# Kernel tuning notes

Hardware: AMD Instinct MI355X
Metric: run time of the kernel (lower is better)

Reference implementation:

```python
import jax, jax.numpy as jnp
import numpy as np
from functools import partial

RED = 128      # reduced_dim
MK = 24        # r2d_m * r2d_k
HD, WD = 32, 16  # depth feature grid after 3 stride-2 convs on 256x128


def _conv(x, w, b):
    # torch Conv2d(k=3, stride=2, padding=1), NCHW / OIHW
    y = jax.lax.conv_general_dilated(
        x, w, window_strides=(2, 2), padding=((1, 1), (1, 1)),
        dimension_numbers=("NCHW", "OIHW", "NCHW"))
    return y + b[None, :, None, None]


def setup_inputs() -> dict:
    key = jax.random.key(0)
    ks = jax.random.split(key, 24)
    B = 64
    s = 0.02
    inp = {
        "features": jax.random.normal(ks[0], (B, 129, 768), jnp.float32),
        "d": jax.random.uniform(ks[1], (B, 1, 256, 128), jnp.float32),
        "W_rg": jax.random.normal(ks[2], (768, RED), jnp.float32) * s,
        "b_rg": jnp.zeros((RED,), jnp.float32),
        "W_rl": jax.random.normal(ks[3], (768, RED), jnp.float32) * s,
        "b_rl": jnp.zeros((RED,), jnp.float32),
        "conv1_w": jax.random.normal(ks[4], (64, 1, 3, 3), jnp.float32) * s,
        "conv1_b": jnp.zeros((64,), jnp.float32),
        "conv2_w": jax.random.normal(ks[5], (128, 64, 3, 3), jnp.float32) * s,
        "conv2_b": jnp.zeros((128,), jnp.float32),
        "conv3_w": jax.random.normal(ks[6], (128, 128, 3, 3), jnp.float32) * s,
        "conv3_b": jnp.zeros((128,), jnp.float32),
        "g_depth": jax.random.normal(ks[7], (RED,), jnp.float32),
        "W_merge": jax.random.normal(ks[8], (2 * RED, RED), jnp.float32) * s,
        "b_merge": jnp.zeros((RED,), jnp.float32),
        "W_q": jax.random.normal(ks[9], (2 * RED, RED), jnp.float32) * s,
        "b_q": jnp.zeros((RED,), jnp.float32),
        "W_v": jax.random.normal(ks[10], (RED, RED), jnp.float32) * s,
        "b_v": jnp.zeros((RED,), jnp.float32),
        "W_sel": jax.random.normal(ks[11], (RED, 3 * MK), jnp.float32) * s,
        "b_sel": jnp.zeros((3 * MK,), jnp.float32),
        "W_cls": jax.random.normal(ks[12], (RED, 751), jnp.float32) * s,
    }
    return inp


def _forward(features, d, W_rg, b_rg, W_rl, b_rl, conv1_w, conv1_b, conv2_w,
             conv2_b, conv3_w, conv3_b, g_depth, W_merge, b_merge, W_q, b_q,
             W_v, b_v, W_sel, b_sel, W_cls):
    B = features.shape[0]
    N = features.shape[1] - 1
    global_feat = features[:, 0] @ W_rg + b_rg                 # (B, 128)
    local_feat = features[:, 1:] @ W_rl + b_rl                 # (B, N, 128)
    lcg = jnp.concatenate(
        [jnp.broadcast_to(global_feat[:, None], (B, N, RED)), local_feat], -1)

    dep = _conv(_conv(_conv(d, conv1_w, conv1_b), conv2_w, conv2_b),
                conv3_w, conv3_b)                              # (B,128,32,16)
    dep = dep.transpose(0, 2, 3, 1).reshape(B, HD * WD, RED)
    lcgd = jnp.concatenate(
        [jnp.broadcast_to(g_depth[None, None], (B, HD * WD, RED)), dep], -1)
    lcgd = lcgd @ W_merge + b_merge

    q = lcg @ W_q + b_q                                        # (B,N,128)
    v = lcgd @ W_v + b_v                                       # (B,512,128)
    sel = jax.nn.sigmoid(q @ W_sel + b_sel)                    # (B,N,72)
    lx = sel[:, :, 0:2 * MK:2]                                 # (B,N,24)
    ly = sel[:, :, 1:2 * MK:2]
    attn = jax.nn.softmax(sel[:, :, 2 * MK:], axis=-1)

    # integer corner grid (original uses // stride == floor(loc*(dim-1)))
    x1 = jnp.floor(lx * (WD - 1))
    x2 = jnp.minimum(x1 + 1.0, float(WD - 1))
    y1 = jnp.floor(ly * (HD - 1))
    y2 = jnp.minimum(y1 + 1.0, float(HD - 1))
    xi1, xi2 = x1.astype(jnp.int32), x2.astype(jnp.int32)
    yi1, yi2 = y1.astype(jnp.int32), y2.astype(jnp.int32)

    # faithful to original gather: index = x_idx * Wd + y_idx
    gather = jax.vmap(lambda vb, ib: vb[ib])                   # (512,C),(N,K)->(N,K,C)
    f0 = gather(v, xi1 * WD + yi2)
    f1 = gather(v, xi2 * WD + yi2)
    f2 = gather(v, xi2 * WD + yi1)
    f3 = gather(v, xi1 * WD + yi1)

    # query coordinates scaled by full grid size (as in the original)
    x = lx * WD
    y = ly * HD
    w_ = x2 - x1
    h_ = y2 - y1
    degenerate = (h_ == 0) | (w_ == 0)
    denom = jnp.where(h_ * w_ == 0, 1.0, h_ * w_)
    coeff = jnp.where(degenerate, 2.0, 1.0 / denom)            # (B,N,24)
    xv0 = jnp.where(w_ == 0, 1.0, x2 - x)
    xv1 = jnp.where(w_ == 0, 1.0, x - x1)
    yv0 = jnp.where(h_ == 0, 1.0, y2 - y)
    yv1 = jnp.where(h_ == 0, 1.0, y - y1)

    # xv^T @ [[f0,f1],[f2,f3]] @ yv, per channel
    interp = coeff[..., None] * (
        xv0[..., None] * (f0 * yv0[..., None] + f1 * yv1[..., None]) +
        xv1[..., None] * (f2 * yv0[..., None] + f3 * yv1[..., None]))

    r2d_feat = jnp.mean(interp * attn[..., None], axis=-2)     # (B,N,128)
    final_embedding = jnp.mean(r2d_feat, axis=1)               # (B,128)
    cls_score = final_embedding @ W_cls                        # (B,751)
    return cls_score, final_embedding


def reference(features, d, W_rg, b_rg, W_rl, b_rl, conv1_w, conv1_b, conv2_w,
              conv2_b, conv3_w, conv3_b, g_depth, W_merge, b_merge, W_q, b_q,
              W_v, b_v, W_sel, b_sel, W_cls):
    return _forward(features, d, W_rg, b_rg, W_rl, b_rl, conv1_w, conv1_b,
                    conv2_w, conv2_b, conv3_w, conv3_b, g_depth, W_merge,
                    b_merge, W_q, b_q, W_v, b_v, W_sel, b_sel, W_cls)
```

## Files before the change

### kernel.cpp

```cpp
#include <hip/hip_runtime.h>
#include <hip/hip_bf16.h>


typedef __attribute__((ext_vector_type(8))) short short8;
typedef __attribute__((ext_vector_type(4))) short shortx4;
typedef __attribute__((ext_vector_type(4))) float floatx4;
typedef __attribute__((ext_vector_type(4))) int intx4;

#define MFMA16(a, b, c) __builtin_amdgcn_mfma_f32_16x16x32_bf16(a, b, c, 0, 0, 0)

__global__ __launch_bounds__(256) void prep_a(
    const float* __restrict__ W_q, const float* __restrict__ W_sel,
    const float* __restrict__ W_merge, const float* __restrict__ W_v,
    const float* __restrict__ g_depth, const float* __restrict__ b_merge,
    const float* __restrict__ features, const float* __restrict__ W_rg,
    const float* __restrict__ b_rg, const float* __restrict__ c2w,
    const float* __restrict__ c3w,
    float* __restrict__ W_qs, float* __restrict__ W_mv,
    float* __restrict__ c0, float* __restrict__ gfeat,
    __hip_bfloat16* __restrict__ w2t, __hip_bfloat16* __restrict__ w3t)
{
    __shared__ float fr_s[768];
    int bid = blockIdx.x, t = threadIdx.x;
    if (bid < 72) {
        int j = bid;
        float acc = 0.f;
        for (int k = 0; k < 128; ++k)
            acc = fmaf(W_q[t * 128 + k], W_sel[k * 72 + j], acc);
        W_qs[t * 72 + j] = acc;
    } else if (bid < 200) {
        int j = bid - 72;
        if (t < 128) {
            float acc = 0.f;
            for (int k = 0; k < 128; ++k)
                acc = fmaf(W_merge[(128 + t) * 128 + k], W_v[k * 128 + j], acc);
            W_mv[t * 128 + j] = acc;
        }
    } else if (bid == 200) {
        if (t < 128) {
            float acc = b_merge[t];
            for (int k = 0; k < 128; ++k)
                acc = fmaf(g_depth[k], W_merge[k * 128 + t], acc);
            c0[t] = acc;
        }
    } else if (bid < 265) {
        int row = bid - 201;
        for (int l = t; l < 768; l += 256)
            fr_s[l] = features[(long)row * 129 * 768 + l];
        __syncthreads();
        if (t < 128) {
            float acc = b_rg[t];
            for (int k = 0; k < 768; ++k)
                acc = fmaf(fr_s[k], W_rg[k * 128 + t], acc);
            gfeat[row * 128 + t] = acc;
        }
    } else if (bid < 553) {
        int idx = (bid - 265) * 256 + t;
        if (idx < 128 * 576) {
            int oc = idx / 576, k = idx % 576;
            int s = k >> 6, ic = k & 63;
            w2t[idx] = __float2bfloat16(c2w[oc * 576 + ic * 9 + s]);
        }
    } else {
        int idx = (bid - 553) * 256 + t;
        if (idx < 128 * 1152) {
            int oc = idx / 1152, k = idx % 1152;
            int s = k >> 7, ic = k & 127;
            w3t[idx] = __float2bfloat16(c3w[oc * 1152 + ic * 9 + s]);
        }
    }
}

__global__ __launch_bounds__(256) void prep2_k(
    const float* __restrict__ W_rl, const float* __restrict__ W_qs,
    const float* __restrict__ W_sel, const float* __restrict__ b_rl,
    const float* __restrict__ b_q, const float* __restrict__ b_sel,
    const float* __restrict__ gfeat, const float* __restrict__ c0,
    const float* __restrict__ W_v, const float* __restrict__ b_v,
    float* __restrict__ W_big, float* __restrict__ rowbias,
    float* __restrict__ c0v)
{
    int bid = blockIdx.x, t = threadIdx.x;
    if (bid < 216) {
        int j = bid / 3;
        int i = (bid % 3) * 256 + t;
        float acc = 0.f;
        for (int k = 0; k < 128; ++k)
            acc = fmaf(W_rl[i * 128 + k], W_qs[(128 + k) * 72 + j], acc);
        W_big[i * 72 + j] = acc;
    } else if (bid < 288) {
        int j = bid - 216;
        if (t < 64) {
            float vb = b_sel[j];
            for (int k = 0; k < 128; ++k) {
                vb = fmaf(b_rl[k], W_qs[(128 + k) * 72 + j], vb);
                vb = fmaf(b_q[k], W_sel[k * 72 + j], vb);
            }
            float acc = vb;
            for (int k = 0; k < 128; ++k)
                acc = fmaf(gfeat[t * 128 + k], W_qs[k * 72 + j], acc);
            rowbias[t * 72 + j] = acc;
        }
    } else {
        if (t < 128) {
            float acc = b_v[t];
            for (int k = 0; k < 128; ++k)
                acc = fmaf(c0[k], W_v[k * 128 + t], acc);
            c0v[t] = acc;
        }
    }
}

__global__ __launch_bounds__(256) void prep_b(
    const float* __restrict__ W_mv, const float* __restrict__ W_big,
    __hip_bfloat16* __restrict__ Bh, __hip_bfloat16* __restrict__ Bl,
    __hip_bfloat16* __restrict__ Wbh, __hip_bfloat16* __restrict__ Wbl)
{
    int bid = blockIdx.x, t = threadIdx.x;
    if (bid < 64) {
        int idx = bid * 256 + t;
        int n = idx >> 7, k = idx & 127;
        float w = W_mv[k * 128 + n];
        __hip_bfloat16 h = __float2bfloat16(w);
        Bh[idx] = h;
        Bl[idx] = __float2bfloat16(w - __bfloat162float(h));
    } else {
        int idx = (bid - 64) * 256 + t;
        if (idx < 80 * 768) {
            int n = idx / 768, k = idx - n * 768;
            float w = (n < 72) ? W_big[k * 72 + n] : 0.f;
            __hip_bfloat16 h = __float2bfloat16(w);
            Wbh[idx] = h;
            Wbl[idx] = __float2bfloat16(w - __bfloat162float(h));
        }
    }
}

__global__ __launch_bounds__(256) void conv1_k(
    const float* __restrict__ d, const float* __restrict__ w,
    const float* __restrict__ bias, __hip_bfloat16* __restrict__ out)
{
    __shared__ float in_s[3][66];
    __shared__ float ws_[576];
    __shared__ float bs_[64];
    int tid = threadIdx.x;
    int owhalf = blockIdx.x & 1;
    int oh = (blockIdx.x >> 1) & 127;
    int b  = blockIdx.x >> 8;
    int owbase = owhalf * 32;

    for (int l = tid; l < 576; l += 256) ws_[l] = w[l];
    if (tid < 64) bs_[tid] = bias[tid];
    for (int l = tid; l < 3 * 66; l += 256) {
        int r = l / 66, c = l % 66;
        int ih = 2 * oh - 1 + r;
        int iw = 2 * owbase - 1 + c;
        float v = 0.f;
        if ((unsigned)ih < 256u && (unsigned)iw < 128u)
            v = d[(b * 256 + ih) * 128 + iw];
        in_s[r][c] = v;
    }
    __syncthreads();

    int owl = tid >> 3, ocg = tid & 7;
    float in9[9];
#pragma unroll
    for (int r = 0; r < 3; ++r)
#pragma unroll
        for (int c = 0; c < 3; ++c)
            in9[r * 3 + c] = in_s[r][2 * owl + c];

    short8 res;
#pragma unroll
    for (int j = 0; j < 8; ++j) {
        int oc = ocg * 8 + j;
        float a = bs_[oc];
#pragma unroll
        for (int s = 0; s < 9; ++s) a = fmaf(in9[s], ws_[oc * 9 + s], a);
        union { __hip_bfloat16 h; short s; } u;
        u.h = __float2bfloat16(a);
        res[j] = u.s;
    }
    long pos = ((long)(b * 128 + oh) * 64 + owbase + owl);
    *(short8*)((short*)out + pos * 64 + ocg * 8) = res;
}

__global__ __launch_bounds__(256) void conv2_mfma(
    const __hip_bfloat16* __restrict__ in, const __hip_bfloat16* __restrict__ w2t,
    const float* __restrict__ bias, __hip_bfloat16* __restrict__ out)
{
    __shared__ short A_lds[128][72];
    __shared__ short B_lds[128][72];
    int tid = threadIdx.x;
    int oh0 = blockIdx.x * 4;
    int b   = blockIdx.y;
    int lane = tid & 63, wave = tid >> 6;
    int l16 = lane & 15, lh = lane >> 4;
    const short* inp = (const short*)in;
    const short* w2p = (const short*)w2t;

    floatx4 acc[2][8] = {};

    for (int s = 0; s < 9; ++s) {
        int kh = s / 3, kw = s - kh * 3;
        short8 av[4], bv[4];
#pragma unroll
        for (int i = 0; i < 4; ++i) {
            int c = tid + i * 256;
            int pos = c >> 3, seg = c & 7;
            int ohl = pos >> 5, ow = pos & 31;
            int ih = 2 * (oh0 + ohl) - 1 + kh;
            int iw = 2 * ow - 1 + kw;
            short8 v = {0,0,0,0,0,0,0,0};
            if ((unsigned)ih < 128u && (unsigned)iw < 64u)
                v = *(const short8*)(inp + (((long)(b * 128 + ih) * 64 + iw) * 64 + seg * 8));
            av[i] = v;
            bv[i] = *(const short8*)(w2p + pos * 576 + s * 64 + seg * 8);
        }
        __syncthreads();
#pragma unroll
        for (int i = 0; i < 4; ++i) {
            int c = tid + i * 256;
            int pos = c >> 3, seg = c & 7;
            *(short8*)&A_lds[pos][seg * 8] = av[i];
            *(short8*)&B_lds[pos][seg * 8] = bv[i];
        }
        __syncthreads();
#pragma unroll
        for (int half = 0; half < 2; ++half) {
            short8 a0 = *(const short8*)&A_lds[wave * 32 + l16][half * 32 + lh * 8];
            short8 a1 = *(const short8*)&A_lds[wave * 32 + 16 + l16][half * 32 + lh * 8];
#pragma unroll
            for (int ni = 0; ni < 8; ++ni) {
                short8 bvf = *(const short8*)&B_lds[ni * 16 + l16][half * 32 + lh * 8];
                acc[0][ni] = MFMA16(a0, bvf, acc[0][ni]);
                acc[1][ni] = MFMA16(a1, bvf, acc[1][ni]);
            }
        }
    }

    float bf[8];
#pragma unroll
    for (int ni = 0; ni < 8; ++ni) bf[ni] = bias[ni * 16 + l16];
#pragma unroll
    for (int mi = 0; mi < 2; ++mi)
#pragma unroll
        for (int r = 0; r < 4; ++r) {
            int m = wave * 32 + mi * 16 + lh * 4 + r;
            int ohl = m >> 5, ow = m & 31;
            __hip_bfloat16* op = out + (((long)(b * 64 + oh0 + ohl) * 32) + ow) * 128;
#pragma unroll
            for (int ni = 0; ni < 8; ++ni) {
                int oc = ni * 16 + l16;
                op[oc] = __float2bfloat16(acc[mi][ni][r] + bf[ni]);
            }
        }
}

__global__ __launch_bounds__(256) void conv3_mfma(
    const __hip_bfloat16* __restrict__ in, const __hip_bfloat16* __restrict__ w3t,
    const float* __restrict__ bias, float* __restrict__ dep)
{
    __shared__ short A_lds[64][136];
    __shared__ short B_lds[128][136];
    int tid = threadIdx.x;
    int oh0 = blockIdx.x * 4;
    int b   = blockIdx.y;
    int lane = tid & 63, wave = tid >> 6;
    int wr = wave >> 1, wc = wave & 1;
    int l16 = lane & 15, lh = lane >> 4;
    const short* inp = (const short*)in;
    const short* w3p = (const short*)w3t;

    floatx4 acc[2][4] = {};

    for (int s = 0; s < 9; ++s) {
        int kh = s / 3, kw = s - kh * 3;
        short8 av[4], bv[8];
#pragma unroll
        for (int i = 0; i < 4; ++i) {
            int c = tid + i * 256;
            int pos = c >> 4, seg = c & 15;
            int oa = pos >> 4, ow = pos & 15;
            int ih = 2 * (oh0 + oa) - 1 + kh;
            int iw = 2 * ow - 1 + kw;
            short8 v = {0,0,0,0,0,0,0,0};
            if ((unsigned)ih < 64u && (unsigned)iw < 32u)
                v = *(const short8*)(inp + (((long)(b * 64 + ih) * 32 + iw) * 128 + seg * 8));
            av[i] = v;
        }
#pragma unroll
        for (int i = 0; i < 8; ++i) {
            int c = tid + i * 256;
            int oc = c >> 4, seg = c & 15;
            bv[i] = *(const short8*)(w3p + oc * 1152 + s * 128 + seg * 8);
        }
        __syncthreads();
#pragma unroll
        for (int i = 0; i < 4; ++i) {
            int c = tid + i * 256;
            int pos = c >> 4, seg = c & 15;
            *(short8*)&A_lds[pos][seg * 8] = av[i];
        }
#pragma unroll
        for (int i = 0; i < 8; ++i) {
            int c = tid + i * 256;
            int oc = c >> 4, seg = c & 15;
            *(short8*)&B_lds[oc][seg * 8] = bv[i];
        }
        __syncthreads();
#pragma unroll
        for (int ks = 0; ks < 4; ++ks) {
            short8 a0 = *(const short8*)&A_lds[wr * 32 + l16][ks * 32 + lh * 8];
            short8 a1 = *(const short8*)&A_lds[wr * 32 + 16 + l16][ks * 32 + lh * 8];
#pragma unroll
            for (int ni = 0; ni < 4; ++ni) {
                short8 bvf = *(const short8*)&B_lds[wc * 64 + ni * 16 + l16][ks * 32 + lh * 8];
                acc[0][ni] = MFMA16(a0, bvf, acc[0][ni]);
                acc[1][ni] = MFMA16(a1, bvf, acc[1][ni]);
            }
        }
    }

    float bf[4];
#pragma unroll
    for (int ni = 0; ni < 4; ++ni) bf[ni] = bias[wc * 64 + ni * 16 + l16];
#pragma unroll
    for (int mi = 0; mi < 2; ++mi)
#pragma unroll
        for (int r = 0; r < 4; ++r) {
            int m = wr * 32 + mi * 16 + lh * 4 + r;
            int oa2 = m >> 4, ow2 = m & 15;
            float* op = dep + ((long)b * 512 + (oh0 + oa2) * 16 + ow2) * 128;
#pragma unroll
            for (int ni = 0; ni < 4; ++ni) {
                int oc = wc * 64 + ni * 16 + l16;
                op[oc] = acc[mi][ni][r] + bf[ni];
            }
        }
}

__global__ __launch_bounds__(256) void vgemm_mfma(
    const float* __restrict__ dep, const __hip_bfloat16* __restrict__ Bh,
    const __hip_bfloat16* __restrict__ Bl, const float* __restrict__ c0v,
    float* __restrict__ v)
{
    __shared__ short Ah[64][136];
    __shared__ short Al[64][136];
    int tid = threadIdx.x;
    int m0 = blockIdx.x * 64;

    for (int l4 = tid; l4 < 64 * 32; l4 += 256) {
        int r = l4 >> 5, c4 = l4 & 31;
        const float* sp = dep + ((long)(m0 + r) << 7) + c4 * 4;
        shortx4 hv, lv;
#pragma unroll
        for (int i = 0; i < 4; ++i) {
            float f = sp[i];
            union { __hip_bfloat16 b; short s; } uh, ul;
            uh.b = __float2bfloat16(f);
            ul.b = __float2bfloat16(f - __bfloat162float(uh.b));
            hv[i] = uh.s; lv[i] = ul.s;
        }
        *(shortx4*)&Ah[r][c4 * 4] = hv;
        *(shortx4*)&Al[r][c4 * 4] = lv;
    }
    __syncthreads();

    int lane = tid & 63, wave = tid >> 6;
    int wr = wave >> 1, wc = wave & 1;
    int l16 = lane & 15, lh = lane >> 4;
    floatx4 acc[2][4] = {};
#pragma unroll
    for (int kk = 0; kk < 4; ++kk) {
        short8 ah[2], al[2];
#pragma unroll
        for (int mi = 0; mi < 2; ++mi) {
            ah[mi] = *(const short8*)&Ah[wr * 32 + mi * 16 + l16][kk * 32 + lh * 8];
            al[mi] = *(const short8*)&Al[wr * 32 + mi * 16 + l16][kk * 32 + lh * 8];
        }
#pragma unroll
        for (int nf = 0; nf < 4; ++nf) {
            int gn = wc * 64 + nf * 16 + l16;
            short8 bh = *(const short8*)((const short*)Bh + gn * 128 + kk * 32 + lh * 8);
            short8 bl = *(const short8*)((const short*)Bl + gn * 128 + kk * 32 + lh * 8);
#pragma unroll
            for (int mi = 0; mi < 2; ++mi) {
                acc[mi][nf] = MFMA16(ah[mi], bh, acc[mi][nf]);
                acc[mi][nf] = MFMA16(al[mi], bh, acc[mi][nf]);
                acc[mi][nf] = MFMA16(ah[mi], bl, acc[mi][nf]);
            }
        }
    }
#pragma unroll
    for (int nf = 0; nf < 4; ++nf) {
        int gn = wc * 64 + nf * 16 + l16;
        float cv = c0v[gn];
#pragma unroll
        for (int mi = 0; mi < 2; ++mi)
#pragma unroll
            for (int r = 0; r < 4; ++r) {
                int m = m0 + wr * 32 + mi * 16 + lh * 4 + r;
                v[(long)m * 128 + gn] = acc[mi][nf][r] + cv;
            }
    }
}

__global__ __launch_bounds__(256) void selbw_k(
    const float* __restrict__ F, const __hip_bfloat16* __restrict__ Wbh,
    const __hip_bfloat16* __restrict__ Wbl, const float* __restrict__ rowbias,
    int* __restrict__ idxb, float* __restrict__ wtb)
{
    __shared__ short Ah[16][136];
    __shared__ short Al[16][136];
    __shared__ float slx[16][24], sly[16][24], satt[16][24];
    int tid = threadIdx.x;
    int m0 = blockIdx.x * 16;
    int padd = (m0 >> 7) + 1;
    int lane = tid & 63, wave = tid >> 6;
    int l16 = lane & 15, lh = lane >> 4;

    int sr = tid >> 4, sc = (tid & 15) * 8;
    const float* fsrc = F + (long)(m0 + sr + padd) * 768 + sc;

    floatx4 acc0 = {0.f, 0.f, 0.f, 0.f};
    floatx4 acc1 = {0.f, 0.f, 0.f, 0.f};
    bool two = (wave == 3);
    const short* bhp = (const short*)Wbh;
    const short* blp = (const short*)Wbl;
    int gn0 = wave * 16 + l16;
    int gn1 = 64 + l16;

    for (int c = 0; c < 6; ++c) {
        __syncthreads();
        float4 f0 = *(const float4*)(fsrc + c * 128);
        float4 f1 = *(const float4*)(fsrc + c * 128 + 4);
        shortx4 h0, l0, h1, l1;
#pragma unroll
        for (int i = 0; i < 4; ++i) {
            union { __hip_bfloat16 b; short s; } uh, ul;
            float fa = (&f0.x)[i];
            uh.b = __float2bfloat16(fa);
            ul.b = __float2bfloat16(fa - __bfloat162float(uh.b));
            h0[i] = uh.s; l0[i] = ul.s;
            float fb = (&f1.x)[i];
            uh.b = __float2bfloat16(fb);
            ul.b = __float2bfloat16(fb - __bfloat162float(uh.b));
            h1[i] = uh.s; l1[i] = ul.s;
        }
        *(shortx4*)&Ah[sr][sc]     = h0;
        *(shortx4*)&Ah[sr][sc + 4] = h1;
        *(shortx4*)&Al[sr][sc]     = l0;
        *(shortx4*)&Al[sr][sc + 4] = l1;
        __syncthreads();
#pragma unroll
        for (int ks = 0; ks < 4; ++ks) {
            short8 ah = *(const short8*)&Ah[l16][ks * 32 + lh * 8];
            short8 al = *(const short8*)&Al[l16][ks * 32 + lh * 8];
            int koff = c * 128 + ks * 32 + lh * 8;
            short8 bh0 = *(const short8*)(bhp + gn0 * 768 + koff);
            short8 bl0 = *(const short8*)(blp + gn0 * 768 + koff);
            acc0 = MFMA16(ah, bh0, acc0);
            acc0 = MFMA16(al, bh0, acc0);
            acc0 = MFMA16(ah, bl0, acc0);
            if (two) {
                short8 bh1 = *(const short8*)(bhp + gn1 * 768 + koff);
                short8 bl1 = *(const short8*)(blp + gn1 * 768 + koff);
                acc1 = MFMA16(ah, bh1, acc1);
                acc1 = MFMA16(al, bh1, acc1);
                acc1 = MFMA16(ah, bl1, acc1);
            }
        }
    }

    if (wave < 3) {
        int j = wave * 16 + l16;
#pragma unroll
        for (int r = 0; r < 4; ++r) {
            int rl = lh * 4 + r;
            float val = acc0[r] + rowbias[((m0 + rl) >> 7) * 72 + j];
            float sg = 1.f / (1.f + expf(-val));
            if (j & 1) sly[rl][j >> 1] = sg;
            else       slx[rl][j >> 1] = sg;
        }
    } else {
#pragma unroll
        for (int r = 0; r < 4; ++r) {
            int rl = lh * 4 + r;
            int b72 = ((m0 + rl) >> 7) * 72;
            float s0 = 1.f / (1.f + expf(-(acc0[r] + rowbias[b72 + 48 + l16])));
            float s1 = -1e30f;
            if (l16 < 8)
                s1 = 1.f / (1.f + expf(-(acc1[r] + rowbias[b72 + 64 + l16])));
            float mx = fmaxf(s0, s1);
#pragma unroll
            for (int s = 1; s < 16; s <<= 1)
                mx = fmaxf(mx, __shfl_xor(mx, s));
            float e0 = expf(s0 - mx);
            float e1 = (l16 < 8) ? expf(s1 - mx) : 0.f;
            float sum = e0 + e1;
#pragma unroll
            for (int s = 1; s < 16; s <<= 1)
                sum += __shfl_xor(sum, s);
            satt[rl][l16] = e0 / sum;
            if (l16 < 8) satt[rl][16 + l16] = e1 / sum;
        }
    }
    __syncthreads();

    for (int e = tid; e < 384; e += 256) {
        int rl = e / 24, k = e - rl * 24;
        int row = m0 + rl;
        float lxv = slx[rl][k], lyv = sly[rl][k];
        float a = satt[rl][k] * (1.f / 24.f);
        float x1 = floorf(lxv * 15.f), x2 = fminf(x1 + 1.f, 15.f);
        float y1 = floorf(lyv * 31.f), y2 = fminf(y1 + 1.f, 31.f);
        int xi1 = (int)x1, xi2 = (int)x2, yi1 = (int)y1, yi2 = (int)y2;
        float x = lxv * 16.f, y = lyv * 32.f;
        float w_ = x2 - x1, h_ = y2 - y1;
        float hwp = h_ * w_;
        bool deg = (h_ == 0.f) || (w_ == 0.f);
        float denom = (hwp == 0.f) ? 1.f : hwp;
        float coeff = (deg ? 2.f : 1.f / denom) * a;
        float xv0 = (w_ == 0.f) ? 1.f : (x2 - x);
        float xv1 = (w_ == 0.f) ? 1.f : (x - x1);
        float yv0 = (h_ == 0.f) ? 1.f : (y2 - y);
        float yv1 = (h_ == 0.f) ? 1.f : (y - y1);
        intx4 iv; floatx4 wv;
        iv[0] = (xi1 * 16 + yi2) * 128;
        iv[1] = (xi2 * 16 + yi2) * 128;
        iv[2] = (xi2 * 16 + yi1) * 128;
        iv[3] = (xi1 * 16 + yi1) * 128;
        wv[0] = coeff * xv0 * yv0;
        wv[1] = coeff * xv0 * yv1;
        wv[2] = coeff * xv1 * yv0;
        wv[3] = coeff * xv1 * yv1;
        *(intx4*)&idxb[(long)row * 96 + k * 4] = iv;
        *(floatx4*)&wtb[(long)row * 96 + k * 4] = wv;
    }
}

__global__ __launch_bounds__(256) void r2d_k(
    const float* __restrict__ v, const int* __restrict__ idxb,
    const float* __restrict__ wtb, float* __restrict__ r2d)
{
    int rg = blockIdx.x;
    int b  = blockIdx.y;
    int tid = threadIdx.x;
    int c  = tid & 127;
    int rp = tid >> 7;
    __shared__ int sidx[8][96];
    __shared__ float swt[8][96];
    for (int l = tid; l < 8 * 96; l += 256) {
        int rr = l / 96, e = l - rr * 96;
        long base = ((long)(b * 128 + rg * 8 + rr)) * 96 + e;
        sidx[rr][e] = idxb[base];
        swt[rr][e]  = wtb[base];
    }
    __syncthreads();
    const float* vb = v + (long)b * 512 * 128 + c;
#pragma unroll
    for (int it = 0; it < 4; ++it) {
        int rr = it * 2 + rp;
        const int* si = sidx[rr];
        const float* sw = swt[rr];
        float acc = 0.f;
#pragma unroll
        for (int k = 0; k < 24; ++k) {
            float v0 = vb[si[k * 4 + 0]];
            float v1 = vb[si[k * 4 + 1]];
            float v2 = vb[si[k * 4 + 2]];
            float v3 = vb[si[k * 4 + 3]];
            acc = fmaf(sw[k * 4 + 0], v0, acc);
            acc = fmaf(sw[k * 4 + 1], v1, acc);
            acc = fmaf(sw[k * 4 + 2], v2, acc);
            acc = fmaf(sw[k * 4 + 3], v3, acc);
        }
        r2d[((long)(b * 128 + rg * 8 + rr)) * 128 + c] = acc;
    }
}

__global__ __launch_bounds__(256) void fecls_k(
    const float* __restrict__ r2d, const float* __restrict__ W_cls,
    float* __restrict__ out)
{
    __shared__ float fe_s[128];
    int b = blockIdx.x, t = threadIdx.x;
    if (t < 128) {
        float acc = 0.f;
        for (int nn = 0; nn < 128; ++nn)
            acc += r2d[((long)b * 128 + nn) * 128 + t];
        acc *= (1.f / 128.f);
        fe_s[t] = acc;
        out[64 * 751 + b * 128 + t] = acc;
    }
    __syncthreads();
    for (int j = t; j < 751; j += 256) {
        float acc = 0.f;
        for (int k = 0; k < 128; ++k)
            acc = fmaf(fe_s[k], W_cls[k * 751 + j], acc);
        out[b * 751 + j] = acc;
    }
}

extern "C" void kernel_launch(void* const* d_in, const int* in_sizes, int n_in,
                              void* d_out, int out_size, void* d_ws, size_t ws_size,
                              hipStream_t stream)
{
    const float* features = (const float*)d_in[0];
    const float* d        = (const float*)d_in[1];
    const float* W_rg  = (const float*)d_in[2];
    const float* b_rg  = (const float*)d_in[3];
    const float* W_rl  = (const float*)d_in[4];
    const float* b_rl  = (const float*)d_in[5];
    const float* c1w   = (const float*)d_in[6];
    const float* c1b   = (const float*)d_in[7];
    const float* c2w   = (const float*)d_in[8];
    const float* c2b   = (const float*)d_in[9];
    const float* c3w   = (const float*)d_in[10];
    const float* c3b   = (const float*)d_in[11];
    const float* g_depth = (const float*)d_in[12];
    const float* W_merge = (const float*)d_in[13];
    const float* b_merge = (const float*)d_in[14];
    const float* W_q   = (const float*)d_in[15];
    const float* b_q   = (const float*)d_in[16];
    const float* W_v   = (const float*)d_in[17];
    const float* b_v   = (const float*)d_in[18];
    const float* W_sel = (const float*)d_in[19];
    const float* b_sel = (const float*)d_in[20];
    const float* W_cls = (const float*)d_in[21];
    float* out = (float*)d_out;

    char* ws = (char*)d_ws;
    __hip_bfloat16* c1 = (__hip_bfloat16*)(ws + 0);
    float* dep    = (float*)(ws + 0);
    float* v      = (float*)(ws + 33554432);
    __hip_bfloat16* c2 = (__hip_bfloat16*)(ws + 67108864);
    __hip_bfloat16* w2t = (__hip_bfloat16*)(ws + 100663296);
    __hip_bfloat16* w3t = (__hip_bfloat16*)(ws + 100810752);
    float* W_qs    = (float*)(ws + 101105664);
    float* W_mv    = (float*)(ws + 101179392);
    float* W_big   = (float*)(ws + 101244928);
    float* rowbias = (float*)(ws + 101466112);
    float* c0b     = (float*)(ws + 101484544);
    float* c0v     = (float*)(ws + 101485056);
    float* gfeat   = (float*)(ws + 101485568);
    __hip_bfloat16* Wmv_bh = (__hip_bfloat16*)(ws + 101518336);
    __hip_bfloat16* Wmv_bl = (__hip_bfloat16*)(ws + 101551104);
    __hip_bfloat16* Wbig_h = (__hip_bfloat16*)(ws + 101583872);
    __hip_bfloat16* Wbig_l = (__hip_bfloat16*)(ws + 101706752);
    int*   idxb   = (int*)(ws + 101832704);
    float* wtb    = (float*)(ws + 104978432);
    float* r2d    = (float*)(ws + 113836544);

    prep_a<<<1129, 256, 0, stream>>>(W_q, W_sel, W_merge, W_v, g_depth, b_merge,
                                     features, W_rg, b_rg, c2w, c3w,
                                     W_qs, W_mv, c0b, gfeat, w2t, w3t);
    prep2_k<<<289, 256, 0, stream>>>(W_rl, W_qs, W_sel, b_rl, b_q, b_sel,
                                     gfeat, c0b, W_v, b_v, W_big, rowbias, c0v);
    prep_b<<<304, 256, 0, stream>>>(W_mv, W_big, Wmv_bh, Wmv_bl, Wbig_h, Wbig_l);

    conv1_k<<<16384, 256, 0, stream>>>(d, c1w, c1b, c1);
    conv2_mfma<<<dim3(16, 64), 256, 0, stream>>>(c1, w2t, c2b, c2);
    conv3_mfma<<<dim3(8, 64), 256, 0, stream>>>(c2, w3t, c3b, dep);

    vgemm_mfma<<<512, 256, 0, stream>>>(dep, Wmv_bh, Wmv_bl, c0v, v);
    selbw_k<<<512, 256, 0, stream>>>(features, Wbig_h, Wbig_l, rowbias,
                                     idxb, wtb);

    r2d_k<<<dim3(16, 64), 256, 0, stream>>>(v, idxb, wtb, r2d);
    fecls_k<<<64, 256, 0, stream>>>(r2d, W_cls, out);
}
```

Measured before the change: 215.9 us.

## Fuse value GEMM into conv3 epilogue and retile conv1 over four rows

The conv3 kernel now writes its biased output into LDS as bf16 hi/lo pairs and runs the split-precision value GEMM on that tile directly, so the separate vgemm kernel and the 32 MB fp32 depth-feature round trip through global memory go away. Separately, conv1 now handles four output rows across the full width per block (2048 blocks instead of 16384), which amortizes the weight and bias staging and reduces block count. The price is longer conv3 blocks with more register pressure and an extra barrier, and conv1 threads that each compute eight positions.

```diff
diff --git a/kernel.cpp b/kernel.cpp
--- a/kernel.cpp
+++ b/kernel.cpp
@@ -140,21 +140,20 @@
     const float* __restrict__ d, const float* __restrict__ w,
     const float* __restrict__ bias, __hip_bfloat16* __restrict__ out)
 {
-    __shared__ float in_s[3][66];
+    __shared__ float in_s[9][130];
     __shared__ float ws_[576];
     __shared__ float bs_[64];
     int tid = threadIdx.x;
-    int owhalf = blockIdx.x & 1;
-    int oh = (blockIdx.x >> 1) & 127;
-    int b  = blockIdx.x >> 8;
-    int owbase = owhalf * 32;
+    int ohg = blockIdx.x & 31;
+    int b   = blockIdx.x >> 5;
+    int oh0 = ohg * 4;
 
     for (int l = tid; l < 576; l += 256) ws_[l] = w[l];
     if (tid < 64) bs_[tid] = bias[tid];
-    for (int l = tid; l < 3 * 66; l += 256) {
-        int r = l / 66, c = l % 66;
-        int ih = 2 * oh - 1 + r;
-        int iw = 2 * owbase - 1 + c;
+    for (int l = tid; l < 9 * 130; l += 256) {
+        int r = l / 130, c = l - r * 130;
+        int ih = 2 * oh0 - 1 + r;
+        int iw = c - 1;
         float v = 0.f;
         if ((unsigned)ih < 256u && (unsigned)iw < 128u)
             v = d[(b * 256 + ih) * 128 + iw];
@@ -162,27 +161,29 @@
     }
     __syncthreads();
 
-    int owl = tid >> 3, ocg = tid & 7;
-    float in9[9];
-#pragma unroll
-    for (int r = 0; r < 3; ++r)
-#pragma unroll
-        for (int c = 0; c < 3; ++c)
-            in9[r * 3 + c] = in_s[r][2 * owl + c];
-
-    short8 res;
-#pragma unroll
-    for (int j = 0; j < 8; ++j) {
-        int oc = ocg * 8 + j;
-        float a = bs_[oc];
-#pragma unroll
-        for (int s = 0; s < 9; ++s) a = fmaf(in9[s], ws_[oc * 9 + s], a);
-        union { __hip_bfloat16 h; short s; } u;
-        u.h = __float2bfloat16(a);
-        res[j] = u.s;
-    }
-    long pos = ((long)(b * 128 + oh) * 64 + owbase + owl);
-    *(short8*)((short*)out + pos * 64 + ocg * 8) = res;
+    int ocg = tid & 7;
+#pragma unroll
+    for (int pb = 0; pb < 8; ++pb) {
+        int pos = pb * 32 + (tid >> 3);
+        int ohl = pos >> 6, ow = pos & 63;
+        short8 res;
+#pragma unroll
+        for (int j = 0; j < 8; ++j) {
+            int oc = ocg * 8 + j;
+            float a = bs_[oc];
+#pragma unroll
+            for (int kh = 0; kh < 3; ++kh)
+#pragma unroll
+                for (int kw = 0; kw < 3; ++kw)
+                    a = fmaf(in_s[2 * ohl + kh][2 * ow + kw],
+                             ws_[oc * 9 + kh * 3 + kw], a);
+            union { __hip_bfloat16 h; short s; } u;
+            u.h = __float2bfloat16(a);
+            res[j] = u.s;
+        }
+        long gpos = ((long)(b * 128 + oh0 + ohl) * 64 + ow);
+        *(short8*)((short*)out + gpos * 64 + ocg * 8) = res;
+    }
 }
 
 __global__ __launch_bounds__(256) void conv2_mfma(
@@ -259,7 +260,9 @@
 
 __global__ __launch_bounds__(256) void conv3_mfma(
     const __hip_bfloat16* __restrict__ in, const __hip_bfloat16* __restrict__ w3t,
-    const float* __restrict__ bias, float* __restrict__ dep)
+    const float* __restrict__ bias, const __hip_bfloat16* __restrict__ Bh,
+    const __hip_bfloat16* __restrict__ Bl, const float* __restrict__ c0v,
+    float* __restrict__ v)
 {
     __shared__ short A_lds[64][136];
     __shared__ short B_lds[128][136];
@@ -284,10 +287,10 @@
             int oa = pos >> 4, ow = pos & 15;
             int ih = 2 * (oh0 + oa) - 1 + kh;
             int iw = 2 * ow - 1 + kw;
-            short8 v = {0,0,0,0,0,0,0,0};
+            short8 vv = {0,0,0,0,0,0,0,0};
             if ((unsigned)ih < 64u && (unsigned)iw < 32u)
-                v = *(const short8*)(inp + (((long)(b * 64 + ih) * 32 + iw) * 128 + seg * 8));
-            av[i] = v;
+                vv = *(const short8*)(inp + (((long)(b * 64 + ih) * 32 + iw) * 128 + seg * 8));
+            av[i] = vv;
         }
 #pragma unroll
         for (int i = 0; i < 8; ++i) {
@@ -325,59 +328,36 @@
     float bf[4];
 #pragma unroll
     for (int ni = 0; ni < 4; ++ni) bf[ni] = bias[wc * 64 + ni * 16 + l16];
+
+    __syncthreads();
+    short (*Dh)[136] = A_lds;
+    short (*Dl)[136] = B_lds;
 #pragma unroll
     for (int mi = 0; mi < 2; ++mi)
 #pragma unroll
         for (int r = 0; r < 4; ++r) {
             int m = wr * 32 + mi * 16 + lh * 4 + r;
-            int oa2 = m >> 4, ow2 = m & 15;
-            float* op = dep + ((long)b * 512 + (oh0 + oa2) * 16 + ow2) * 128;
 #pragma unroll
             for (int ni = 0; ni < 4; ++ni) {
                 int oc = wc * 64 + ni * 16 + l16;
-                op[oc] = acc[mi][ni][r] + bf[ni];
-            }
-        }
-}
-
-__global__ __launch_bounds__(256) void vgemm_mfma(
-    const float* __restrict__ dep, const __hip_bfloat16* __restrict__ Bh,
-    const __hip_bfloat16* __restrict__ Bl, const float* __restrict__ c0v,
-    float* __restrict__ v)
-{
-    __shared__ short Ah[64][136];
-    __shared__ short Al[64][136];
-    int tid = threadIdx.x;
-    int m0 = blockIdx.x * 64;
-
-    for (int l4 = tid; l4 < 64 * 32; l4 += 256) {
-        int r = l4 >> 5, c4 = l4 & 31;
-        const float* sp = dep + ((long)(m0 + r) << 7) + c4 * 4;
-        shortx4 hv, lv;
-#pragma unroll
-        for (int i = 0; i < 4; ++i) {
-            float f = sp[i];
-            union { __hip_bfloat16 b; short s; } uh, ul;
-            uh.b = __float2bfloat16(f);
-            ul.b = __float2bfloat16(f - __bfloat162float(uh.b));
-            hv[i] = uh.s; lv[i] = ul.s;
-        }
-        *(shortx4*)&Ah[r][c4 * 4] = hv;
-        *(shortx4*)&Al[r][c4 * 4] = lv;
-    }
+                float f = acc[mi][ni][r] + bf[ni];
+                union { __hip_bfloat16 bb; short ss; } uh, ul;
+                uh.bb = __float2bfloat16(f);
+                ul.bb = __float2bfloat16(f - __bfloat162float(uh.bb));
+                Dh[m][oc] = uh.ss;
+                Dl[m][oc] = ul.ss;
+            }
+        }
     __syncthreads();
 
-    int lane = tid & 63, wave = tid >> 6;
-    int wr = wave >> 1, wc = wave & 1;
-    int l16 = lane & 15, lh = lane >> 4;
-    floatx4 acc[2][4] = {};
+    floatx4 vacc[2][4] = {};
 #pragma unroll
     for (int kk = 0; kk < 4; ++kk) {
         short8 ah[2], al[2];
 #pragma unroll
         for (int mi = 0; mi < 2; ++mi) {
-            ah[mi] = *(const short8*)&Ah[wr * 32 + mi * 16 + l16][kk * 32 + lh * 8];
-            al[mi] = *(const short8*)&Al[wr * 32 + mi * 16 + l16][kk * 32 + lh * 8];
+            ah[mi] = *(const short8*)&Dh[wr * 32 + mi * 16 + l16][kk * 32 + lh * 8];
+            al[mi] = *(const short8*)&Dl[wr * 32 + mi * 16 + l16][kk * 32 + lh * 8];
         }
 #pragma unroll
         for (int nf = 0; nf < 4; ++nf) {
@@ -386,9 +366,9 @@
             short8 bl = *(const short8*)((const short*)Bl + gn * 128 + kk * 32 + lh * 8);
 #pragma unroll
             for (int mi = 0; mi < 2; ++mi) {
-                acc[mi][nf] = MFMA16(ah[mi], bh, acc[mi][nf]);
-                acc[mi][nf] = MFMA16(al[mi], bh, acc[mi][nf]);
-                acc[mi][nf] = MFMA16(ah[mi], bl, acc[mi][nf]);
+                vacc[mi][nf] = MFMA16(ah[mi], bh, vacc[mi][nf]);
+                vacc[mi][nf] = MFMA16(al[mi], bh, vacc[mi][nf]);
+                vacc[mi][nf] = MFMA16(ah[mi], bl, vacc[mi][nf]);
             }
         }
     }
@@ -400,8 +380,8 @@
         for (int mi = 0; mi < 2; ++mi)
 #pragma unroll
             for (int r = 0; r < 4; ++r) {
-                int m = m0 + wr * 32 + mi * 16 + lh * 4 + r;
-                v[(long)m * 128 + gn] = acc[mi][nf][r] + cv;
+                int m = wr * 32 + mi * 16 + lh * 4 + r;
+                v[((long)(b * 512 + oh0 * 16 + m)) * 128 + gn] = vacc[mi][nf][r] + cv;
             }
     }
 }
@@ -633,7 +613,6 @@
 
     char* ws = (char*)d_ws;
     __hip_bfloat16* c1 = (__hip_bfloat16*)(ws + 0);
-    float* dep    = (float*)(ws + 0);
     float* v      = (float*)(ws + 33554432);
     __hip_bfloat16* c2 = (__hip_bfloat16*)(ws + 67108864);
     __hip_bfloat16* w2t = (__hip_bfloat16*)(ws + 100663296);
@@ -660,11 +639,11 @@
                                      gfeat, c0b, W_v, b_v, W_big, rowbias, c0v);
     prep_b<<<304, 256, 0, stream>>>(W_mv, W_big, Wmv_bh, Wmv_bl, Wbig_h, Wbig_l);
 
-    conv1_k<<<16384, 256, 0, stream>>>(d, c1w, c1b, c1);
+    conv1_k<<<2048, 256, 0, stream>>>(d, c1w, c1b, c1);
     conv2_mfma<<<dim3(16, 64), 256, 0, stream>>>(c1, w2t, c2b, c2);
-    conv3_mfma<<<dim3(8, 64), 256, 0, stream>>>(c2, w3t, c3b, dep);
-
-    vgemm_mfma<<<512, 256, 0, stream>>>(dep, Wmv_bh, Wmv_bl, c0v, v);
+    conv3_mfma<<<dim3(8, 64), 256, 0, stream>>>(c2, w3t, c3b,
+                                                Wmv_bh, Wmv_bl, c0v, v);
+
     selbw_k<<<512, 256, 0, stream>>>(features, Wbig_h, Wbig_l, rowbias,
                                      idxb, wtb);
 
```

Result: faster. 207.7 us (-3.8%).
